# Performance work log

Hardware: AMD Instinct MI355X
Metric: run time of the kernel (lower is better)

## Reference

```python
import jax, jax.numpy as jnp
import numpy as np

G = 16  # self.group
K = 3   # unfold/fold kernel size


def setup_inputs() -> dict:
    key = jax.random.key(0)
    feature = jax.random.normal(key, (2, 128, 192, 192), dtype=jnp.float32)
    return {"feature": feature}


def reference(feature):
    B, C, H, W = feature.shape
    Cg = C // G
    Hm, Wm = H - K + 1, W - K + 1
    L = Hm * Wm

    # --- nn.Unfold(kernel_size=3), all groups at once ---
    # patches[b, c, k, y, x] with k = ki*3 + kj (channel-major flat = c*9 + k)
    slices = [feature[:, :, ki:ki + Hm, kj:kj + Wm] for ki in range(K) for kj in range(K)]
    patches = jnp.stack(slices, axis=2)                 # [B, C, 9, Hm, Wm]
    # per-group series flat dim is Cg*9 (order cg*9+k); chunk(9) -> reshape [9, Cg]
    motif = patches.reshape(B, G, Cg * 9, L).reshape(B, G, 9, Cg, L)  # [B,G,9,Cg,L]

    # --- cdist + diag=inf + argmin (squared distances: same argmin as p=2) ---
    gram = jnp.einsum('bgjcl,bgjdl->bgjcd', motif, motif)   # [B,G,9,Cg,Cg]
    sq = jnp.einsum('bgjcl,bgjcl->bgjc', motif, motif)      # [B,G,9,Cg]
    d2 = sq[..., :, None] + sq[..., None, :] - 2.0 * gram
    eye = jnp.eye(Cg, dtype=bool)
    d2 = jnp.where(eye, jnp.inf, d2)
    nn_idx = jnp.argmin(d2, axis=-1)                        # [B,G,9,Cg] int

    # --- torch.unique loop overwrites motif_new: only the LAST (max) unique
    # index and its count survive ---
    u_max = jnp.max(nn_idx, axis=-1)                        # [B,G,9]
    c_max = jnp.sum(nn_idx == u_max[..., None], axis=-1).astype(feature.dtype)  # [B,G,9]

    motif_nn = jnp.take_along_axis(motif, u_max[..., None, None], axis=3)  # [B,G,9,1,L]
    # float '//' in torch is floor division
    term = jnp.floor(motif * motif_nn * c_max[..., None, None] / Cg)
    # l == 0 branch drops the '+ motif' term
    batch_mask = (jnp.arange(B) != 0).astype(feature.dtype).reshape(B, 1, 1, 1, 1)
    out_ser = motif * batch_mask + term                     # [B,G,9,Cg,L]

    # --- nn.Fold: input layout reinterpreted as (channel, kernel) flat = c*9+k ---
    ser2 = out_ser.reshape(B, G, 9 * Cg, L).reshape(B, G, Cg, 9, Hm, Wm)
    out = jnp.zeros((B, G, Cg, H, W), feature.dtype)
    for k in range(K * K):
        ki, kj = k // K, k % K
        out = out.at[:, :, :, ki:ki + Hm, kj:kj + Wm].add(ser2[:, :, :, k])
    return out.reshape(B, C, H, W)
```

## Files before the change

kernel.cpp:

```cpp
#include <hip/hip_runtime.h>
#include <hip/hip_bf16.h>
#include <math.h>

#define BB 2
#define CC 128
#define GG 16
#define CG 8
#define HH 192
#define WW 192
#define HM 190
#define WM 190
#define LL (HM * WM)
#define HWSZ (HH * WW)
#define NTRIPLE (BB * GG * 9)

__device__ int g_rel[BB * GG * 72];
__device__ float g_scl[BB * GG * 72];

__global__ __launch_bounds__(1024) void phase1_kernel(
    const float* __restrict__ feat) {
  const int bid = blockIdx.x;
  const int b = bid / (GG * 9);
  const int rem = bid % (GG * 9);
  const int g = rem / 9;
  const int j = rem % 9;

  const float* base[8];
#pragma unroll
  for (int d = 0; d < 8; ++d) {
    const int f = j * 8 + d;
    const int c = f / 9;
    const int k = f % 9;
    const int ki = k / 3, kj = k % 3;
    base[d] = feat + (size_t)(b * CC + g * CG + c) * HWSZ + ki * WW + kj;
  }

  float sq[8];
  float gram[28];
#pragma unroll
  for (int i = 0; i < 8; ++i) sq[i] = 0.0f;
#pragma unroll
  for (int i = 0; i < 28; ++i) gram[i] = 0.0f;

  for (int l = threadIdx.x; l < LL; l += 1024) {
    const int y = l / WM;
    const int x = l - y * WM;
    const int off = y * WW + x;
    float v[8];
#pragma unroll
    for (int d = 0; d < 8; ++d) v[d] = base[d][off];
#pragma unroll
    for (int d = 0; d < 8; ++d) sq[d] += v[d] * v[d];
    int p = 0;
#pragma unroll
    for (int c = 0; c < 8; ++c)
#pragma unroll
      for (int d = c + 1; d < 8; ++d) gram[p++] += v[c] * v[d];
  }

  __shared__ float red[36 * 16];
  __shared__ float tot[36];
  const int lane = threadIdx.x & 63;
  const int wave = threadIdx.x >> 6;
#pragma unroll
  for (int i = 0; i < 8; ++i) {
    float v = sq[i];
    for (int o = 32; o > 0; o >>= 1) v += __shfl_down(v, o, 64);
    if (lane == 0) red[i * 16 + wave] = v;
  }
#pragma unroll
  for (int i = 0; i < 28; ++i) {
    float v = gram[i];
    for (int o = 32; o > 0; o >>= 1) v += __shfl_down(v, o, 64);
    if (lane == 0) red[(8 + i) * 16 + wave] = v;
  }
  __syncthreads();
  if (threadIdx.x < 36) {
    float s = 0.0f;
#pragma unroll
    for (int t = 0; t < 16; ++t) s += red[threadIdx.x * 16 + t];
    tot[threadIdx.x] = s;
  }
  __syncthreads();

  if (threadIdx.x == 0) {
    float s[8], gm[8][8];
    for (int i = 0; i < 8; ++i) s[i] = tot[i];
    int p = 0;
    for (int c = 0; c < 8; ++c)
      for (int d = c + 1; d < 8; ++d) {
        gm[c][d] = tot[8 + p];
        gm[d][c] = tot[8 + p];
        ++p;
      }
    int nn[8];
    for (int c = 0; c < 8; ++c) {
      float best = INFINITY;
      int bi = 0;
      for (int d = 0; d < 8; ++d) {
        if (d == c) continue;
        const float d2 = s[c] + s[d] - 2.0f * gm[c][d];
        if (d2 < best) {
          best = d2;
          bi = d;
        }
      }
      nn[c] = bi;
    }
    int um = 0;
    for (int c = 0; c < 8; ++c) um = um > nn[c] ? um : nn[c];
    int cnt = 0;
    for (int c = 0; c < 8; ++c) cnt += (nn[c] == um) ? 1 : 0;

    const float sc = (float)cnt * 0.125f;
    const int fn = j * 8 + um;
    const int cn = fn / 9;
    const int kn = fn % 9;
    const int kin = kn / 3, kjn = kn % 3;
    for (int d = 0; d < 8; ++d) {
      const int f = j * 8 + d;
      const int cl = f / 9;
      const int k = f % 9;
      const int ki = k / 3, kj = k % 3;
      const int rel = (cn - cl) * HWSZ + (kin - ki) * WW + (kjn - kj);
      const int tix = (b * GG + g) * 72 + f;
      g_rel[tix] = rel;
      g_scl[tix] = sc;
    }
  }
}

__global__ __launch_bounds__(256) void phase2_kernel(
    const float* __restrict__ feat, float* __restrict__ out) {
  const int BLOCKS_PER_PLANE = HWSZ / 256;
  const int plane = blockIdx.x / BLOCKS_PER_PLANE;
  const int within = blockIdx.x % BLOCKS_PER_PLANE;
  const int b = plane / CC;
  const int ch = plane % CC;
  const int g = ch >> 3;
  const int cl = ch & 7;

  const int pix = within * 256 + (int)threadIdx.x;
  const int h = pix / WW;
  const int w = pix % WW;
  const int idx = plane * HWSZ + pix;

  const int tbase = (b * GG + g) * 72 + cl * 9;
  int off[9];
  float scl[9];
#pragma unroll
  for (int k = 0; k < 9; ++k) {
    off[k] = g_rel[tbase + k];
    scl[k] = g_scl[tbase + k];
  }

  const float v = feat[idx];
  const float* basep = feat + idx;
  float acc = 0.0f;
  int nv = 0;
#pragma unroll
  for (int k = 0; k < 9; ++k) {
    const int ki = k / 3, kj = k % 3;
    const bool valid = (h >= ki) & (h < HM + ki) & (w >= kj) & (w < WM + kj);
    const int o = valid ? off[k] : 0;
    const float vn = basep[o];
    float tv = v * vn;
    tv = tv * scl[k];
    const float fl = floorf(tv);
    acc += valid ? fl : 0.0f;
    nv += valid ? 1 : 0;
  }
  if (b != 0) acc += (float)nv * v;
  out[idx] = acc;
}

extern "C" void kernel_launch(void* const* d_in, const int* in_sizes, int n_in,
                              void* d_out, int out_size, void* d_ws,
                              size_t ws_size, hipStream_t stream) {
  const float* feat = (const float*)d_in[0];
  float* out = (float*)d_out;
  (void)d_ws;
  (void)ws_size;

  phase1_kernel<<<NTRIPLE, 1024, 0, stream>>>(feat);

  const int total = BB * CC * HWSZ;
  phase2_kernel<<<total / 256, 256, 0, stream>>>(feat, out);
}
```

Baseline: 153.7 us.

## Split Gram reduction across blocks and process rows per wavefront in phase2

The per-triple Gram/norm reduction is split into six slices handled by separate 256-thread blocks, which write partials to a global buffer. A new small kernel sums the partials and does the nearest-neighbour/argmin selection. This raises phase-1 parallelism from 288 large blocks to 1728 smaller ones, at the cost of an extra launch. Phase 2 is restructured so each wavefront handles a full image row, three pixels per lane, and loads offsets and scales only for valid kernel rows. Fold counts are computed in closed form rather than accumulated per tap.

```diff
diff --git a/kernel.cpp b/kernel.cpp
--- a/kernel.cpp
+++ b/kernel.cpp
@@ -13,15 +13,19 @@
 #define LL (HM * WM)
 #define HWSZ (HH * WW)
 #define NTRIPLE (BB * GG * 9)
-
+#define SPLIT 6
+#define SLICE_LEN ((LL + SPLIT - 1) / SPLIT)
+
+__device__ float g_part[NTRIPLE * SPLIT * 36];
 __device__ int g_rel[BB * GG * 72];
 __device__ float g_scl[BB * GG * 72];
 
-__global__ __launch_bounds__(1024) void phase1_kernel(
+__global__ __launch_bounds__(256) void phase1a_kernel(
     const float* __restrict__ feat) {
-  const int bid = blockIdx.x;
-  const int b = bid / (GG * 9);
-  const int rem = bid % (GG * 9);
+  const int tri = blockIdx.x / SPLIT;
+  const int sl = blockIdx.x % SPLIT;
+  const int b = tri / (GG * 9);
+  const int rem = tri % (GG * 9);
   const int g = rem / 9;
   const int j = rem % 9;
 
@@ -35,14 +39,13 @@
     base[d] = feat + (size_t)(b * CC + g * CG + c) * HWSZ + ki * WW + kj;
   }
 
-  float sq[8];
-  float gram[28];
-#pragma unroll
-  for (int i = 0; i < 8; ++i) sq[i] = 0.0f;
-#pragma unroll
-  for (int i = 0; i < 28; ++i) gram[i] = 0.0f;
-
-  for (int l = threadIdx.x; l < LL; l += 1024) {
+  float acc[36];
+#pragma unroll
+  for (int i = 0; i < 36; ++i) acc[i] = 0.0f;
+
+  const int l0 = sl * SLICE_LEN;
+  const int l1 = (l0 + SLICE_LEN < LL) ? (l0 + SLICE_LEN) : LL;
+  for (int l = l0 + (int)threadIdx.x; l < l1; l += 256) {
     const int y = l / WM;
     const int x = l - y * WM;
     const int off = y * WW + x;
@@ -50,128 +53,150 @@
 #pragma unroll
     for (int d = 0; d < 8; ++d) v[d] = base[d][off];
 #pragma unroll
-    for (int d = 0; d < 8; ++d) sq[d] += v[d] * v[d];
-    int p = 0;
+    for (int d = 0; d < 8; ++d) acc[d] += v[d] * v[d];
+    int p = 8;
 #pragma unroll
     for (int c = 0; c < 8; ++c)
 #pragma unroll
-      for (int d = c + 1; d < 8; ++d) gram[p++] += v[c] * v[d];
-  }
-
-  __shared__ float red[36 * 16];
-  __shared__ float tot[36];
+      for (int d = c + 1; d < 8; ++d) acc[p++] += v[c] * v[d];
+  }
+
+  __shared__ float red[36 * 4];
   const int lane = threadIdx.x & 63;
   const int wave = threadIdx.x >> 6;
 #pragma unroll
-  for (int i = 0; i < 8; ++i) {
-    float v = sq[i];
+  for (int i = 0; i < 36; ++i) {
+    float v = acc[i];
     for (int o = 32; o > 0; o >>= 1) v += __shfl_down(v, o, 64);
-    if (lane == 0) red[i * 16 + wave] = v;
-  }
-#pragma unroll
-  for (int i = 0; i < 28; ++i) {
-    float v = gram[i];
-    for (int o = 32; o > 0; o >>= 1) v += __shfl_down(v, o, 64);
-    if (lane == 0) red[(8 + i) * 16 + wave] = v;
+    if (lane == 0) red[i * 4 + wave] = v;
   }
   __syncthreads();
   if (threadIdx.x < 36) {
-    float s = 0.0f;
-#pragma unroll
-    for (int t = 0; t < 16; ++t) s += red[threadIdx.x * 16 + t];
-    tot[threadIdx.x] = s;
-  }
-  __syncthreads();
-
-  if (threadIdx.x == 0) {
-    float s[8], gm[8][8];
-    for (int i = 0; i < 8; ++i) s[i] = tot[i];
-    int p = 0;
+    const int i = threadIdx.x;
+    g_part[(tri * SPLIT + sl) * 36 + i] =
+        red[i * 4] + red[i * 4 + 1] + red[i * 4 + 2] + red[i * 4 + 3];
+  }
+}
+
+__global__ __launch_bounds__(64) void phase1b_kernel() {
+  const int tri = blockIdx.x * 64 + (int)threadIdx.x;
+  if (tri >= NTRIPLE) return;
+  const int b = tri / (GG * 9);
+  const int rem = tri % (GG * 9);
+  const int g = rem / 9;
+  const int j = rem % 9;
+
+  float tot[36];
+#pragma unroll
+  for (int i = 0; i < 36; ++i) tot[i] = 0.0f;
+  for (int s = 0; s < SPLIT; ++s)
+#pragma unroll
+    for (int i = 0; i < 36; ++i) tot[i] += g_part[(tri * SPLIT + s) * 36 + i];
+
+  float sq[8], gm[8][8];
+#pragma unroll
+  for (int i = 0; i < 8; ++i) sq[i] = tot[i];
+  {
+    int p = 8;
     for (int c = 0; c < 8; ++c)
       for (int d = c + 1; d < 8; ++d) {
-        gm[c][d] = tot[8 + p];
-        gm[d][c] = tot[8 + p];
+        gm[c][d] = tot[p];
+        gm[d][c] = tot[p];
         ++p;
       }
-    int nn[8];
-    for (int c = 0; c < 8; ++c) {
-      float best = INFINITY;
-      int bi = 0;
-      for (int d = 0; d < 8; ++d) {
-        if (d == c) continue;
-        const float d2 = s[c] + s[d] - 2.0f * gm[c][d];
-        if (d2 < best) {
-          best = d2;
-          bi = d;
-        }
+  }
+  int nn[8];
+  for (int c = 0; c < 8; ++c) {
+    float best = INFINITY;
+    int bi = 0;
+    for (int d = 0; d < 8; ++d) {
+      if (d == c) continue;
+      const float d2 = sq[c] + sq[d] - 2.0f * gm[c][d];
+      if (d2 < best) {
+        best = d2;
+        bi = d;
       }
-      nn[c] = bi;
     }
-    int um = 0;
-    for (int c = 0; c < 8; ++c) um = um > nn[c] ? um : nn[c];
-    int cnt = 0;
-    for (int c = 0; c < 8; ++c) cnt += (nn[c] == um) ? 1 : 0;
-
-    const float sc = (float)cnt * 0.125f;
-    const int fn = j * 8 + um;
-    const int cn = fn / 9;
-    const int kn = fn % 9;
-    const int kin = kn / 3, kjn = kn % 3;
-    for (int d = 0; d < 8; ++d) {
-      const int f = j * 8 + d;
-      const int cl = f / 9;
-      const int k = f % 9;
-      const int ki = k / 3, kj = k % 3;
-      const int rel = (cn - cl) * HWSZ + (kin - ki) * WW + (kjn - kj);
-      const int tix = (b * GG + g) * 72 + f;
-      g_rel[tix] = rel;
-      g_scl[tix] = sc;
-    }
+    nn[c] = bi;
+  }
+  int um = 0;
+  for (int c = 0; c < 8; ++c) um = um > nn[c] ? um : nn[c];
+  int cnt = 0;
+  for (int c = 0; c < 8; ++c) cnt += (nn[c] == um) ? 1 : 0;
+
+  const float sc = (float)cnt * 0.125f;
+  const int fn = j * 8 + um;
+  const int cn = fn / 9;
+  const int kn = fn % 9;
+  const int kin = kn / 3, kjn = kn % 3;
+  for (int d = 0; d < 8; ++d) {
+    const int f = j * 8 + d;
+    const int cl = f / 9;
+    const int k = f % 9;
+    const int ki = k / 3, kj = k % 3;
+    const int rel = (cn - cl) * HWSZ + (kin - ki) * WW + (kjn - kj);
+    const int tix = (b * GG + g) * 72 + f;
+    g_rel[tix] = rel;
+    g_scl[tix] = sc;
   }
 }
 
 __global__ __launch_bounds__(256) void phase2_kernel(
     const float* __restrict__ feat, float* __restrict__ out) {
-  const int BLOCKS_PER_PLANE = HWSZ / 256;
-  const int plane = blockIdx.x / BLOCKS_PER_PLANE;
-  const int within = blockIdx.x % BLOCKS_PER_PLANE;
+  const int row = blockIdx.x * 4 + ((int)threadIdx.x >> 6);
+  const int lane = (int)threadIdx.x & 63;
+  const int plane = row / HH;
+  const int h = row % HH;
   const int b = plane / CC;
   const int ch = plane % CC;
   const int g = ch >> 3;
   const int cl = ch & 7;
 
-  const int pix = within * 256 + (int)threadIdx.x;
-  const int h = pix / WW;
-  const int w = pix % WW;
-  const int idx = plane * HWSZ + pix;
-
   const int tbase = (b * GG + g) * 72 + cl * 9;
-  int off[9];
-  float scl[9];
-#pragma unroll
-  for (int k = 0; k < 9; ++k) {
-    off[k] = g_rel[tbase + k];
-    scl[k] = g_scl[tbase + k];
-  }
-
-  const float v = feat[idx];
-  const float* basep = feat + idx;
-  float acc = 0.0f;
-  int nv = 0;
+  const float* rowp = feat + (size_t)plane * HWSZ + h * WW;
+  float* orow = out + (size_t)plane * HWSZ + h * WW;
+  const float* rowlane = rowp + lane;
+
+  const float v0 = rowlane[0];
+  const float v1 = rowlane[64];
+  const float v2 = rowlane[128];
+  float a0 = 0.0f, a1 = 0.0f, a2 = 0.0f;
+
 #pragma unroll
   for (int k = 0; k < 9; ++k) {
     const int ki = k / 3, kj = k % 3;
-    const bool valid = (h >= ki) & (h < HM + ki) & (w >= kj) & (w < WM + kj);
-    const int o = valid ? off[k] : 0;
-    const float vn = basep[o];
-    float tv = v * vn;
-    tv = tv * scl[k];
-    const float fl = floorf(tv);
-    acc += valid ? fl : 0.0f;
-    nv += valid ? 1 : 0;
-  }
-  if (b != 0) acc += (float)nv * v;
-  out[idx] = acc;
+    const bool hv = (h >= ki) & (h < HM + ki);
+    if (hv) {
+      const int oo = g_rel[tbase + k];
+      const float sc = g_scl[tbase + k];
+      const bool wv0 = (lane >= kj);
+      const bool wv2 = (lane < 62 + kj);
+      const int o0 = wv0 ? oo : 0;
+      const int o2 = wv2 ? oo : 0;
+      const float n0 = rowlane[o0];
+      const float n1 = rowlane[oo + 64];
+      const float n2 = rowlane[o2 + 128];
+      const float t0 = floorf(v0 * n0 * sc);
+      const float t1 = floorf(v1 * n1 * sc);
+      const float t2 = floorf(v2 * n2 * sc);
+      a0 += wv0 ? t0 : 0.0f;
+      a1 += t1;
+      a2 += wv2 ? t2 : 0.0f;
+    }
+  }
+
+  if (b != 0) {
+    const int chn = (h < 2 ? h : 2) - (h > 189 ? h - 189 : 0) + 1;
+    const int w0 = lane, w2 = lane + 128;
+    const int cw0 = (w0 < 2 ? w0 : 2) + 1;
+    const int cw2 = 3 - (w2 > 189 ? w2 - 189 : 0);
+    a0 += (float)(chn * cw0) * v0;
+    a1 += (float)(chn * 3) * v1;
+    a2 += (float)(chn * cw2) * v2;
+  }
+  orow[0 + lane] = a0;
+  orow[64 + lane] = a1;
+  orow[128 + lane] = a2;
 }
 
 extern "C" void kernel_launch(void* const* d_in, const int* in_sizes, int n_in,
@@ -182,8 +207,9 @@
   (void)d_ws;
   (void)ws_size;
 
-  phase1_kernel<<<NTRIPLE, 1024, 0, stream>>>(feat);
-
-  const int total = BB * CC * HWSZ;
-  phase2_kernel<<<total / 256, 256, 0, stream>>>(feat, out);
-}
+  phase1a_kernel<<<NTRIPLE * SPLIT, 256, 0, stream>>>(feat);
+  phase1b_kernel<<<(NTRIPLE + 63) / 64, 64, 0, stream>>>();
+
+  const int rows = BB * CC * HH;
+  phase2_kernel<<<rows / 4, 256, 0, stream>>>(feat, out);
+}
```

Measured after the change: 145.7 us. 5.2% less time.
